# Kernel optimization log

Hardware: AMD Instinct MI355X
Metric: run time of the kernel (lower is better)

Reference implementation:

```python
import jax, jax.numpy as jnp
import numpy as np

COST_CLASS, COST_BBOX, COST_GIOU = 1.0, 5.0, 2.0


def box_cxcywh_to_xyxy(b):
    cx, cy, w, h = b[..., 0], b[..., 1], b[..., 2], b[..., 3]
    return jnp.stack([cx - 0.5 * w, cy - 0.5 * h, cx + 0.5 * w, cy + 0.5 * h], axis=-1)


def generalized_box_iou(boxes1, boxes2):
    # boxes1: [N,4], boxes2: [M,4], xyxy -> [N,M] GIoU
    area1 = (boxes1[:, 2] - boxes1[:, 0]) * (boxes1[:, 3] - boxes1[:, 1])  # [N]
    area2 = (boxes2[:, 2] - boxes2[:, 0]) * (boxes2[:, 3] - boxes2[:, 1])  # [M]
    lt = jnp.maximum(boxes1[:, None, :2], boxes2[None, :, :2])  # [N,M,2]
    rb = jnp.minimum(boxes1[:, None, 2:], boxes2[None, :, 2:])
    wh = jnp.clip(rb - lt, 0.0)
    inter = wh[..., 0] * wh[..., 1]                             # [N,M]
    union = area1[:, None] + area2[None, :] - inter
    iou = inter / union
    # smallest enclosing box
    lt_e = jnp.minimum(boxes1[:, None, :2], boxes2[None, :, :2])
    rb_e = jnp.maximum(boxes1[:, None, 2:], boxes2[None, :, 2:])
    wh_e = jnp.clip(rb_e - lt_e, 0.0)
    area_e = wh_e[..., 0] * wh_e[..., 1]
    return iou - (area_e - union) / area_e


def setup_inputs() -> dict:
    key = jax.random.key(0)
    k1, k2, k3, k4 = jax.random.split(key, 4)
    bs, nq, nc, nt = 16, 900, 151, 100
    pred_logits = jax.random.normal(k1, (bs, nq, nc), dtype=jnp.float32)
    # cxcywh boxes with positive extents, well inside [0,1]
    pred_boxes = jax.random.uniform(k2, (bs, nq, 4), dtype=jnp.float32, minval=0.05, maxval=0.5)
    tgt_labels = jax.random.randint(k3, (bs, nt), 0, nc)
    tgt_boxes = jax.random.uniform(k4, (bs, nt, 4), dtype=jnp.float32, minval=0.05, maxval=0.5)
    return {"pred_logits": pred_logits, "pred_boxes": pred_boxes,
            "tgt_labels": tgt_labels, "tgt_boxes": tgt_boxes}


def reference(pred_logits, pred_boxes, tgt_labels, tgt_boxes):
    bs, nq, nc = pred_logits.shape
    out_prob = jax.nn.softmax(pred_logits.reshape(bs * nq, nc), axis=-1)  # [bs*nq, C]
    out_bbox = pred_boxes.reshape(bs * nq, 4)
    tgt_ids = tgt_labels.reshape(-1)          # [T] (all targets concatenated, as in torch.cat)
    tgt_bbox = tgt_boxes.reshape(-1, 4)       # [T, 4]
    cost_class = -out_prob[:, tgt_ids]                                     # [bs*nq, T]
    cost_bbox = jnp.abs(out_bbox[:, None, :] - tgt_bbox[None, :, :]).sum(-1)  # L1 cdist
    cost_giou = -generalized_box_iou(box_cxcywh_to_xyxy(out_bbox), box_cxcywh_to_xyxy(tgt_bbox))
    C = COST_BBOX * cost_bbox + COST_CLASS * cost_class + COST_GIOU * cost_giou
    return C.reshape(bs, nq, -1)  # [bs, nq, T]; per-image split/Hungarian happens on host
```

## Files before the change

### kernel.cpp

```cpp
#include <hip/hip_runtime.h>
#include <math.h>

#define NROWS 14400
#define NT    1600
#define NC    151
#define ROWS_PER_BLOCK 32

__global__ __launch_bounds__(256) void row_prep(
    const float* __restrict__ logits,
    const float* __restrict__ pboxes,
    float* __restrict__ rowdata)
{
    const int wave = threadIdx.x >> 6;
    const int lane = threadIdx.x & 63;
    const int r = blockIdx.x * 4 + wave;

    const float* row = logits + (size_t)r * NC;
    float v0 = row[lane];
    float v1 = row[lane + 64];
    float v2 = (lane < NC - 128) ? row[lane + 128] : -3.4e38f;

    float m = fmaxf(fmaxf(v0, v1), v2);
    #pragma unroll
    for (int off = 32; off; off >>= 1) m = fmaxf(m, __shfl_xor(m, off, 64));

    float s = __expf(v0 - m) + __expf(v1 - m) +
              ((lane < NC - 128) ? __expf(v2 - m) : 0.0f);
    #pragma unroll
    for (int off = 32; off; off >>= 1) s += __shfl_xor(s, off, 64);

    if (lane == 0) {
        float4 pb = ((const float4*)pboxes)[r];
        float x0 = pb.x - 0.5f * pb.z, y0 = pb.y - 0.5f * pb.w;
        float x1 = pb.x + 0.5f * pb.z, y1 = pb.y + 0.5f * pb.w;
        float area = (x1 - x0) * (y1 - y0);
        float* o = rowdata + (size_t)r * 12;
        ((float4*)o)[0] = make_float4(pb.x, pb.y, pb.z, pb.w);
        ((float4*)o)[1] = make_float4(x0, y0, x1, y1);
        ((float4*)o)[2] = make_float4(area, m, 1.0f / s, 0.0f);
    }
}

__global__ __launch_bounds__(320) void cost_kernel(
    const float* __restrict__ logits,
    const int*   __restrict__ tlabels,
    const float* __restrict__ tboxes,
    const float* __restrict__ rowdata,
    float* __restrict__ out)
{
    const int t = blockIdx.x * 320 + threadIdx.x;

    float4 tb = ((const float4*)tboxes)[t];
    const int label = tlabels[t];
    const float tx0 = tb.x - 0.5f * tb.z, ty0 = tb.y - 0.5f * tb.w;
    const float tx1 = tb.x + 0.5f * tb.z, ty1 = tb.y + 0.5f * tb.w;
    const float tarea = (tx1 - tx0) * (ty1 - ty0);

    const int r0 = blockIdx.y * ROWS_PER_BLOCK;
    #pragma unroll 4
    for (int i = 0; i < ROWS_PER_BLOCK; ++i) {
        const int r = r0 + i;
        const float4* rd = (const float4*)(rowdata + (size_t)r * 12);
        const float4 pb  = rd[0];
        const float4 pxy = rd[1];
        const float4 ps  = rd[2];

        const float lg  = logits[(size_t)r * NC + label];
        const float cls = __expf(lg - ps.y) * ps.z;

        const float l1 = fabsf(pb.x - tb.x) + fabsf(pb.y - tb.y) +
                         fabsf(pb.z - tb.z) + fabsf(pb.w - tb.w);

        const float iw = fmaxf(fminf(pxy.z, tx1) - fmaxf(pxy.x, tx0), 0.0f);
        const float ih = fmaxf(fminf(pxy.w, ty1) - fmaxf(pxy.y, ty0), 0.0f);
        const float inter = iw * ih;
        const float uni   = ps.x + tarea - inter;
        const float iou   = inter * __builtin_amdgcn_rcpf(uni);
        const float ew = fmaxf(fmaxf(pxy.z, tx1) - fminf(pxy.x, tx0), 0.0f);
        const float eh = fmaxf(fmaxf(pxy.w, ty1) - fminf(pxy.y, ty0), 0.0f);
        const float earea = ew * eh;
        const float giou  = iou - (earea - uni) * __builtin_amdgcn_rcpf(earea);

        out[(size_t)r * NT + t] = 5.0f * l1 - cls - 2.0f * giou;
    }
}

extern "C" void kernel_launch(void* const* d_in, const int* in_sizes, int n_in,
                              void* d_out, int out_size, void* d_ws, size_t ws_size,
                              hipStream_t stream) {
    const float* logits  = (const float*)d_in[0];
    const float* pboxes  = (const float*)d_in[1];
    const int*   tlabels = (const int*)d_in[2];
    const float* tboxes  = (const float*)d_in[3];
    float* out = (float*)d_out;
    float* rowdata = (float*)d_ws;

    row_prep<<<dim3(NROWS / 4), 256, 0, stream>>>(logits, pboxes, rowdata);
    cost_kernel<<<dim3(5, NROWS / ROWS_PER_BLOCK), 320, 0, stream>>>(
        logits, tlabels, tboxes, rowdata, out);
}
```

Measured before the change: 130.6 us.

## Precompute softmax probabilities and stage per-block rows in shared memory

The row prep kernel now writes the normalized softmax probabilities to workspace. The cost kernel stages its 32 rows of probabilities and box data in LDS, then does a shared-memory lookup per target label instead of a scattered global logit gather plus exp. The redundant clamp on the enclosing box is also dropped. This adds a full probability write and read (about 8.7MB) and a barrier, and falls back to the old path when the workspace is too small.

```diff
diff --git a/kernel.cpp b/kernel.cpp
--- a/kernel.cpp
+++ b/kernel.cpp
@@ -4,12 +4,17 @@
 #define NROWS 14400
 #define NT    1600
 #define NC    151
-#define ROWS_PER_BLOCK 32
+#define RPB   32
+
+#define ROWDATA_BYTES (NROWS * 12 * 4)
+#define PROB_BYTES    ((size_t)NROWS * NC * 4)
+#define WS_NEEDED     (ROWDATA_BYTES + PROB_BYTES)
 
 __global__ __launch_bounds__(256) void row_prep(
     const float* __restrict__ logits,
     const float* __restrict__ pboxes,
-    float* __restrict__ rowdata)
+    float* __restrict__ rowdata,
+    float* __restrict__ prob)
 {
     const int wave = threadIdx.x >> 6;
     const int lane = threadIdx.x & 63;
@@ -24,10 +29,19 @@
     #pragma unroll
     for (int off = 32; off; off >>= 1) m = fmaxf(m, __shfl_xor(m, off, 64));
 
-    float s = __expf(v0 - m) + __expf(v1 - m) +
-              ((lane < NC - 128) ? __expf(v2 - m) : 0.0f);
+    float e0 = __expf(v0 - m), e1 = __expf(v1 - m);
+    float e2 = (lane < NC - 128) ? __expf(v2 - m) : 0.0f;
+    float s = e0 + e1 + e2;
     #pragma unroll
     for (int off = 32; off; off >>= 1) s += __shfl_xor(s, off, 64);
+    const float rinv = 1.0f / s;
+
+    if (prob) {
+        float* pr = prob + (size_t)r * NC;
+        pr[lane]      = e0 * rinv;
+        pr[lane + 64] = e1 * rinv;
+        if (lane < NC - 128) pr[lane + 128] = e2 * rinv;
+    }
 
     if (lane == 0) {
         float4 pb = ((const float4*)pboxes)[r];
@@ -37,11 +51,66 @@
         float* o = rowdata + (size_t)r * 12;
         ((float4*)o)[0] = make_float4(pb.x, pb.y, pb.z, pb.w);
         ((float4*)o)[1] = make_float4(x0, y0, x1, y1);
-        ((float4*)o)[2] = make_float4(area, m, 1.0f / s, 0.0f);
+        ((float4*)o)[2] = make_float4(area, m, rinv, 0.0f);
     }
 }
 
 __global__ __launch_bounds__(320) void cost_kernel(
+    const int*   __restrict__ tlabels,
+    const float* __restrict__ tboxes,
+    const float* __restrict__ rowdata,
+    const float* __restrict__ prob,
+    float* __restrict__ out)
+{
+    __shared__ float sprob[RPB * NC];
+    __shared__ float srow[RPB * 12];
+
+    const int tid = threadIdx.x;
+    const int r0 = blockIdx.y * RPB;
+
+    const float* gp = prob + (size_t)r0 * NC;
+    for (int i = tid; i < RPB * NC; i += 320) sprob[i] = gp[i];
+    const float* gr = rowdata + (size_t)r0 * 12;
+    for (int i = tid; i < RPB * 12; i += 320) srow[i] = gr[i];
+
+    const int t = blockIdx.x * 320 + tid;
+    const float4 tb = ((const float4*)tboxes)[t];
+    const int label = tlabels[t];
+    const float tx0 = tb.x - 0.5f * tb.z, ty0 = tb.y - 0.5f * tb.w;
+    const float tx1 = tb.x + 0.5f * tb.z, ty1 = tb.y + 0.5f * tb.w;
+    const float tarea = (tx1 - tx0) * (ty1 - ty0);
+
+    __syncthreads();
+
+    size_t oaddr = (size_t)r0 * NT + t;
+    #pragma unroll 4
+    for (int i = 0; i < RPB; ++i) {
+        const float4* rd = (const float4*)(srow + i * 12);
+        const float4 pb  = rd[0];
+        const float4 pxy = rd[1];
+        const float  parea = rd[2].x;
+
+        const float cls = sprob[i * NC + label];
+
+        const float l1 = fabsf(pb.x - tb.x) + fabsf(pb.y - tb.y) +
+                         fabsf(pb.z - tb.z) + fabsf(pb.w - tb.w);
+
+        const float iw = fmaxf(fminf(pxy.z, tx1) - fmaxf(pxy.x, tx0), 0.0f);
+        const float ih = fmaxf(fminf(pxy.w, ty1) - fmaxf(pxy.y, ty0), 0.0f);
+        const float inter = iw * ih;
+        const float uni   = parea + tarea - inter;
+        const float iou   = inter * __builtin_amdgcn_rcpf(uni);
+        const float ew = fmaxf(pxy.z, tx1) - fminf(pxy.x, tx0);
+        const float eh = fmaxf(pxy.w, ty1) - fminf(pxy.y, ty0);
+        const float earea = ew * eh;
+        const float giou  = iou - (earea - uni) * __builtin_amdgcn_rcpf(earea);
+
+        out[oaddr] = 5.0f * l1 - cls - 2.0f * giou;
+        oaddr += NT;
+    }
+}
+
+__global__ __launch_bounds__(320) void cost_kernel_fb(
     const float* __restrict__ logits,
     const int*   __restrict__ tlabels,
     const float* __restrict__ tboxes,
@@ -49,38 +118,33 @@
     float* __restrict__ out)
 {
     const int t = blockIdx.x * 320 + threadIdx.x;
-
     float4 tb = ((const float4*)tboxes)[t];
     const int label = tlabels[t];
     const float tx0 = tb.x - 0.5f * tb.z, ty0 = tb.y - 0.5f * tb.w;
     const float tx1 = tb.x + 0.5f * tb.z, ty1 = tb.y + 0.5f * tb.w;
     const float tarea = (tx1 - tx0) * (ty1 - ty0);
 
-    const int r0 = blockIdx.y * ROWS_PER_BLOCK;
+    const int r0 = blockIdx.y * RPB;
     #pragma unroll 4
-    for (int i = 0; i < ROWS_PER_BLOCK; ++i) {
+    for (int i = 0; i < RPB; ++i) {
         const int r = r0 + i;
         const float4* rd = (const float4*)(rowdata + (size_t)r * 12);
         const float4 pb  = rd[0];
         const float4 pxy = rd[1];
         const float4 ps  = rd[2];
-
         const float lg  = logits[(size_t)r * NC + label];
         const float cls = __expf(lg - ps.y) * ps.z;
-
         const float l1 = fabsf(pb.x - tb.x) + fabsf(pb.y - tb.y) +
                          fabsf(pb.z - tb.z) + fabsf(pb.w - tb.w);
-
         const float iw = fmaxf(fminf(pxy.z, tx1) - fmaxf(pxy.x, tx0), 0.0f);
         const float ih = fmaxf(fminf(pxy.w, ty1) - fmaxf(pxy.y, ty0), 0.0f);
         const float inter = iw * ih;
         const float uni   = ps.x + tarea - inter;
         const float iou   = inter * __builtin_amdgcn_rcpf(uni);
-        const float ew = fmaxf(fmaxf(pxy.z, tx1) - fminf(pxy.x, tx0), 0.0f);
-        const float eh = fmaxf(fmaxf(pxy.w, ty1) - fminf(pxy.y, ty0), 0.0f);
+        const float ew = fmaxf(pxy.z, tx1) - fminf(pxy.x, tx0);
+        const float eh = fmaxf(pxy.w, ty1) - fminf(pxy.y, ty0);
         const float earea = ew * eh;
         const float giou  = iou - (earea - uni) * __builtin_amdgcn_rcpf(earea);
-
         out[(size_t)r * NT + t] = 5.0f * l1 - cls - 2.0f * giou;
     }
 }
@@ -94,8 +158,15 @@
     const float* tboxes  = (const float*)d_in[3];
     float* out = (float*)d_out;
     float* rowdata = (float*)d_ws;
+    float* prob = (float*)((char*)d_ws + ROWDATA_BYTES);
 
-    row_prep<<<dim3(NROWS / 4), 256, 0, stream>>>(logits, pboxes, rowdata);
-    cost_kernel<<<dim3(5, NROWS / ROWS_PER_BLOCK), 320, 0, stream>>>(
-        logits, tlabels, tboxes, rowdata, out);
+    if (ws_size >= WS_NEEDED) {
+        row_prep<<<dim3(NROWS / 4), 256, 0, stream>>>(logits, pboxes, rowdata, prob);
+        cost_kernel<<<dim3(5, NROWS / RPB), 320, 0, stream>>>(
+            tlabels, tboxes, rowdata, prob, out);
+    } else {
+        row_prep<<<dim3(NROWS / 4), 256, 0, stream>>>(logits, pboxes, rowdata, nullptr);
+        cost_kernel_fb<<<dim3(5, NROWS / RPB), 320, 0, stream>>>(
+            logits, tlabels, tboxes, rowdata, out);
+    }
 }
```

After: 135.7 us. +3.9%, slower.

## Fuse softmax row prep into cost kernel with shared-memory probability tiles

Applied to the files above, without the earlier changes.

Merges the two kernels into one. Each block now loads its 32 logit rows into LDS, computes the full softmax there, and reads the class probability for each target's label from LDS instead of doing a strided global gather plus an exp per output. This removes one launch, the rowdata workspace round-trip and the scattered global label lookups. In exchange, every one of the 5 column blocks recomputes the softmax for the same rows, and the LDS footprint (about 20KB per block) may reduce occupancy. It also drops the redundant clamp on the enclosing-box width and height.

```diff
diff --git a/kernel.cpp b/kernel.cpp
--- a/kernel.cpp
+++ b/kernel.cpp
@@ -4,69 +4,76 @@
 #define NROWS 14400
 #define NT    1600
 #define NC    151
-#define ROWS_PER_BLOCK 32
+#define RPB   32
+#define TPB   320
+#define QUADS ((RPB * NC) / 4)
 
-__global__ __launch_bounds__(256) void row_prep(
+__global__ __launch_bounds__(TPB) void matcher_fused(
     const float* __restrict__ logits,
     const float* __restrict__ pboxes,
-    float* __restrict__ rowdata)
+    const int*   __restrict__ tlabels,
+    const float* __restrict__ tboxes,
+    float* __restrict__ out)
 {
-    const int wave = threadIdx.x >> 6;
-    const int lane = threadIdx.x & 63;
-    const int r = blockIdx.x * 4 + wave;
+    __shared__ __align__(16) float sprob[RPB * NC];
+    __shared__ __align__(16) float srow[RPB * 12];
 
-    const float* row = logits + (size_t)r * NC;
-    float v0 = row[lane];
-    float v1 = row[lane + 64];
-    float v2 = (lane < NC - 128) ? row[lane + 128] : -3.4e38f;
+    const int tid  = threadIdx.x;
+    const int r0   = blockIdx.y * RPB;
+    const int wave = tid >> 6;
+    const int lane = tid & 63;
 
-    float m = fmaxf(fmaxf(v0, v1), v2);
-    #pragma unroll
-    for (int off = 32; off; off >>= 1) m = fmaxf(m, __shfl_xor(m, off, 64));
-
-    float s = __expf(v0 - m) + __expf(v1 - m) +
-              ((lane < NC - 128) ? __expf(v2 - m) : 0.0f);
-    #pragma unroll
-    for (int off = 32; off; off >>= 1) s += __shfl_xor(s, off, 64);
-
-    if (lane == 0) {
-        float4 pb = ((const float4*)pboxes)[r];
+    {
+        const float4* g4 = (const float4*)(logits + (size_t)r0 * NC);
+        float4* s4 = (float4*)sprob;
+        for (int i = tid; i < QUADS; i += TPB) s4[i] = g4[i];
+    }
+    if (tid < RPB) {
+        float4 pb = ((const float4*)pboxes)[r0 + tid];
         float x0 = pb.x - 0.5f * pb.z, y0 = pb.y - 0.5f * pb.w;
         float x1 = pb.x + 0.5f * pb.z, y1 = pb.y + 0.5f * pb.w;
-        float area = (x1 - x0) * (y1 - y0);
-        float* o = rowdata + (size_t)r * 12;
-        ((float4*)o)[0] = make_float4(pb.x, pb.y, pb.z, pb.w);
+        float* o = srow + tid * 12;
+        ((float4*)o)[0] = pb;
         ((float4*)o)[1] = make_float4(x0, y0, x1, y1);
-        ((float4*)o)[2] = make_float4(area, m, 1.0f / s, 0.0f);
+        o[8] = (x1 - x0) * (y1 - y0);
     }
-}
-
-__global__ __launch_bounds__(320) void cost_kernel(
-    const float* __restrict__ logits,
-    const int*   __restrict__ tlabels,
-    const float* __restrict__ tboxes,
-    const float* __restrict__ rowdata,
-    float* __restrict__ out)
-{
-    const int t = blockIdx.x * 320 + threadIdx.x;
-
-    float4 tb = ((const float4*)tboxes)[t];
+    const int t = blockIdx.x * TPB + tid;
+    const float4 tb = ((const float4*)tboxes)[t];
     const int label = tlabels[t];
     const float tx0 = tb.x - 0.5f * tb.z, ty0 = tb.y - 0.5f * tb.w;
     const float tx1 = tb.x + 0.5f * tb.z, ty1 = tb.y + 0.5f * tb.w;
     const float tarea = (tx1 - tx0) * (ty1 - ty0);
 
-    const int r0 = blockIdx.y * ROWS_PER_BLOCK;
+    __syncthreads();
+
+    for (int i = wave; i < RPB; i += TPB / 64) {
+        float* row = sprob + i * NC;
+        float v0 = row[lane];
+        float v1 = row[lane + 64];
+        float v2 = (lane < NC - 128) ? row[lane + 128] : -3.4e38f;
+        float m = fmaxf(fmaxf(v0, v1), v2);
+        #pragma unroll
+        for (int off = 32; off; off >>= 1) m = fmaxf(m, __shfl_xor(m, off, 64));
+        float e0 = __expf(v0 - m), e1 = __expf(v1 - m);
+        float e2 = (lane < NC - 128) ? __expf(v2 - m) : 0.0f;
+        float s = e0 + e1 + e2;
+        #pragma unroll
+        for (int off = 32; off; off >>= 1) s += __shfl_xor(s, off, 64);
+        const float rinv = 1.0f / s;
+        row[lane]      = e0 * rinv;
+        row[lane + 64] = e1 * rinv;
+        if (lane < NC - 128) row[lane + 128] = e2 * rinv;
+    }
+    __syncthreads();
+
+    size_t oaddr = (size_t)r0 * NT + t;
     #pragma unroll 4
-    for (int i = 0; i < ROWS_PER_BLOCK; ++i) {
-        const int r = r0 + i;
-        const float4* rd = (const float4*)(rowdata + (size_t)r * 12);
-        const float4 pb  = rd[0];
-        const float4 pxy = rd[1];
-        const float4 ps  = rd[2];
+    for (int i = 0; i < RPB; ++i) {
+        const float4 pb  = *(const float4*)(srow + i * 12);
+        const float4 pxy = *(const float4*)(srow + i * 12 + 4);
+        const float parea = srow[i * 12 + 8];
 
-        const float lg  = logits[(size_t)r * NC + label];
-        const float cls = __expf(lg - ps.y) * ps.z;
+        const float cls = sprob[i * NC + label];
 
         const float l1 = fabsf(pb.x - tb.x) + fabsf(pb.y - tb.y) +
                          fabsf(pb.z - tb.z) + fabsf(pb.w - tb.w);
@@ -74,14 +81,15 @@
         const float iw = fmaxf(fminf(pxy.z, tx1) - fmaxf(pxy.x, tx0), 0.0f);
         const float ih = fmaxf(fminf(pxy.w, ty1) - fmaxf(pxy.y, ty0), 0.0f);
         const float inter = iw * ih;
-        const float uni   = ps.x + tarea - inter;
+        const float uni   = parea + tarea - inter;
         const float iou   = inter * __builtin_amdgcn_rcpf(uni);
-        const float ew = fmaxf(fmaxf(pxy.z, tx1) - fminf(pxy.x, tx0), 0.0f);
-        const float eh = fmaxf(fmaxf(pxy.w, ty1) - fminf(pxy.y, ty0), 0.0f);
+        const float ew = fmaxf(pxy.z, tx1) - fminf(pxy.x, tx0);
+        const float eh = fmaxf(pxy.w, ty1) - fminf(pxy.y, ty0);
         const float earea = ew * eh;
         const float giou  = iou - (earea - uni) * __builtin_amdgcn_rcpf(earea);
 
-        out[(size_t)r * NT + t] = 5.0f * l1 - cls - 2.0f * giou;
+        out[oaddr] = 5.0f * l1 - cls - 2.0f * giou;
+        oaddr += NT;
     }
 }
 
@@ -93,9 +101,8 @@
     const int*   tlabels = (const int*)d_in[2];
     const float* tboxes  = (const float*)d_in[3];
     float* out = (float*)d_out;
-    float* rowdata = (float*)d_ws;
+    (void)d_ws; (void)ws_size; (void)out_size; (void)in_sizes; (void)n_in;
 
-    row_prep<<<dim3(NROWS / 4), 256, 0, stream>>>(logits, pboxes, rowdata);
-    cost_kernel<<<dim3(5, NROWS / ROWS_PER_BLOCK), 320, 0, stream>>>(
-        logits, tlabels, tboxes, rowdata, out);
+    matcher_fused<<<dim3(NT / TPB, NROWS / RPB), TPB, 0, stream>>>(
+        logits, pboxes, tlabels, tboxes, out);
 }
```

After: 138.6 us. 6.1% more time.
